# Kernel tuning notes

Hardware: AMD Instinct MI355X
Metric: run time of the kernel (lower is better)

Reference implementation:

```python
import jax, jax.numpy as jnp
import numpy as np

B, C, H, W = 4, 128, 100, 256
M = 2

def setup_inputs() -> dict:
    key = jax.random.key(0)
    ks = jax.random.split(key, 5)
    feat0 = jax.random.normal(ks[0], (B, C, H, W), jnp.float32)
    feat1 = jax.random.normal(ks[1], (B, C, H, W), jnp.float32)
    adapter_weight = jax.random.normal(ks[2], (M, C), jnp.float32)
    # conv: 1x1 Conv2d(M*C -> C); store as [C_out, C_in]
    conv_w = jax.random.normal(ks[3], (C, M * C), jnp.float32) * (1.0 / np.sqrt(M * C))
    conv_b = jnp.zeros((C,), jnp.float32)
    mlp_w = jax.random.normal(ks[4], (C, C), jnp.float32) * (1.0 / np.sqrt(C))
    mlp_b = jnp.zeros((C,), jnp.float32)
    return {"feat0": feat0, "feat1": feat1, "adapter_weight": adapter_weight,
            "conv_w": conv_w, "conv_b": conv_b, "mlp_w": mlp_w, "mlp_b": mlp_b}

def reference(feat0, feat1, adapter_weight, conv_w, conv_b, mlp_w, mlp_b):
    feats = jnp.stack([feat0, feat1], axis=0)              # [M, B, C, H, W]
    b, c, h, w = feat0.shape
    # per-modality scalar-per-channel scale, then concat on channel dim
    scaled = feats * adapter_weight[:, None, :, None, None]
    cat = scaled.transpose(1, 0, 2, 3, 4).reshape(b, -1, h, w)  # [B, M*C, H, W]
    # 1x1 conv == channel matmul
    fused = jnp.einsum('bkhw,ck->bchw', cat, conv_w) + conv_b[None, :, None, None]
    f = fused.transpose(2, 3, 0, 1).reshape(h * w, b, c)   # [(HW), B, C]
    fm = feats.transpose(0, 3, 4, 1, 2).reshape(len(feats), h * w, b, c)  # [M, (HW), B, C]
    # per-location cross-agent attention, summed over modalities
    scores = jnp.einsum('msbc,sdc->msbd', fm, f) / np.sqrt(c).astype(jnp.float32)
    attn = jax.nn.softmax(scores, axis=-1)                 # [M, (HW), B, B]
    retrieved = jnp.einsum('msbd,sdc->sbc', attn, f)       # summed over m
    out = f + jax.nn.relu(retrieved @ mlp_w.T + mlp_b)
    return out.reshape(h, w, b, c).transpose(2, 3, 0, 1)   # [B, C, H, W]
```

## Files before the change

kernel.cpp:

```cpp
#include <hip/hip_runtime.h>

#define HW 25600
#define TS 16
#define NT 1600
#define NB 256

typedef float  f32x4   __attribute__((ext_vector_type(4)));
typedef short  short8  __attribute__((ext_vector_type(8)));
typedef short  short4v __attribute__((ext_vector_type(4)));
typedef unsigned int uint2v __attribute__((ext_vector_type(2)));
typedef unsigned int uint4v __attribute__((ext_vector_type(4)));

__device__ __forceinline__ float bf2f(short h) {
    return __builtin_bit_cast(float, (unsigned)((unsigned short)h) << 16);
}
__device__ __forceinline__ unsigned cvt_pk(float a, float b) {
    unsigned r;
    asm("v_cvt_pk_bf16_f32 %0, %1, %2" : "=v"(r) : "v"(a), "v"(b));
    return r;
}

typedef __attribute__((address_space(3))) const char lds_cchar;
typedef __attribute__((address_space(3))) char lds_char;
typedef __attribute__((address_space(1))) const void g_cvoid;
__device__ __forceinline__ unsigned lds_u32(const void* p) {
    return (unsigned)(uintptr_t)(lds_cchar*)p;
}
__device__ __forceinline__ void dma16(const float* g, unsigned lds_byte) {
    __builtin_amdgcn_global_load_lds(
        (g_cvoid*)g,
        (__attribute__((address_space(3))) void*)(lds_char*)(uintptr_t)lds_byte,
        16, 0, 0);
}

__device__ __forceinline__ short4v tr_read(unsigned a) {
    short4v d;
    asm volatile("ds_read_b64_tr_b16 %0, %1" : "=v"(d) : "v"(a) : "memory");
    return d;
}
__device__ __forceinline__ short4v tr_read128(unsigned a) {
    short4v d;
    asm volatile("ds_read_b64_tr_b16 %0, %1 offset:128" : "=v"(d) : "v"(a) : "memory");
    return d;
}
__device__ __forceinline__ uint4v lds_b128(unsigned a) {
    uint4v d;
    asm volatile("ds_read_b128 %0, %1" : "=v"(d) : "v"(a) : "memory");
    return d;
}
__device__ __forceinline__ void wait_lgkm8() {
    asm volatile("s_waitcnt lgkmcnt(8)" ::: "memory");
    __builtin_amdgcn_sched_barrier(0);
}
__device__ __forceinline__ void wait_lgkm6() {
    asm volatile("s_waitcnt lgkmcnt(6)" ::: "memory");
    __builtin_amdgcn_sched_barrier(0);
}
__device__ __forceinline__ void wait_lgkm4() {
    asm volatile("s_waitcnt lgkmcnt(4)" ::: "memory");
    __builtin_amdgcn_sched_barrier(0);
}
__device__ __forceinline__ void wait_lgkm0() {
    asm volatile("s_waitcnt lgkmcnt(0)" ::: "memory");
    __builtin_amdgcn_sched_barrier(0);
}
__device__ __forceinline__ void wait_vm0() {
    asm volatile("s_waitcnt vmcnt(0)" ::: "memory");
    __builtin_amdgcn_sched_barrier(0);
}
__device__ __forceinline__ void bar_lgkm() {
    asm volatile("s_waitcnt lgkmcnt(0)" ::: "memory");
    __builtin_amdgcn_s_barrier();
    asm volatile("" ::: "memory");
}

struct Clu { short4v lo0, hi0, lo1, hi1, lo2, hi2, lo3, hi3; };
__device__ __forceinline__ void issue_clu(Clu& C, unsigned base, int tstride) {
    C.lo0 = tr_read(base);                C.hi0 = tr_read128(base);
    C.lo1 = tr_read(base + tstride);      C.hi1 = tr_read128(base + tstride);
    C.lo2 = tr_read(base + 2 * tstride);  C.hi2 = tr_read128(base + 2 * tstride);
    C.lo3 = tr_read(base + 3 * tstride);  C.hi3 = tr_read128(base + 3 * tstride);
}
__device__ __forceinline__ short8 mk8(short4v lo, short4v hi) {
    return __builtin_shufflevector(lo, hi, 0, 1, 2, 3, 4, 5, 6, 7);
}

__global__ __launch_bounds__(512, 2) void mmf_kernel(
    const float* __restrict__ feat0, const float* __restrict__ feat1,
    const float* __restrict__ adapter, const float* __restrict__ conv_w,
    const float* __restrict__ conv_b, const float* __restrict__ mlp_w,
    const float* __restrict__ mlp_b, float* __restrict__ out)
{
    __shared__ __align__(128) char smem[133120];
    float* Xf32 = (float*)smem;
    short* Xbf  = (short*)(smem + 65536);
    short* fbf  = (short*)(smem + 98304);
    short* Rbf  = (short*)(smem + 114688);
    float* sc   = (float*)(smem + 131072);

    const int tid = threadIdx.x;
    const int bid = blockIdx.x;
    const int xcd  = bid & 7;
    const int jb   = bid >> 3;
    const int tbeg = 200 * xcd + jb;
    const int tend = 200 * (xcd + 1);
    const int w   = __builtin_amdgcn_readfirstlane(tid >> 6);
    const int l   = tid & 63;
    const int g   = l >> 4;
    const int sl  = l & 15;
    const int c0  = w * 16;

    const unsigned xfbase = lds_u32(Xf32);
    const unsigned xbase  = lds_u32(Xbf);
    const unsigned rbase  = lds_u32(Rbf);

    auto stage_dma = [&](int S) {
        #pragma unroll
        for (int i = 0; i < 8; ++i) {
            int idx = i * 512 + tid;
            int q  = idx & 3;
            int r  = idx >> 2;
            int cc = r & 127;
            int b  = (r >> 7) & 3;
            int m  = r >> 9;
            const float* fp = m ? feat1 : feat0;
            dma16(fp + (size_t)((b * 128 + cc) * HW + S + q * 4),
                  xfbase + (unsigned)((i * 512 + (w << 6)) << 4));
        }
    };

    stage_dma(tbeg * TS);

    short8 afc[8];
    #pragma unroll
    for (int ks = 0; ks < 8; ++ks) {
        const int k0 = ks * 32 + g * 8;
        const float4 w0 = *reinterpret_cast<const float4*>(conv_w + (c0 + sl) * 256 + k0);
        const float4 w1 = *reinterpret_cast<const float4*>(conv_w + (c0 + sl) * 256 + k0 + 4);
        const float4 a0 = *reinterpret_cast<const float4*>(adapter + k0);
        const float4 a1 = *reinterpret_cast<const float4*>(adapter + k0 + 4);
        uint4v au;
        au[0] = cvt_pk(w0.x * a0.x, w0.y * a0.y);
        au[1] = cvt_pk(w0.z * a0.z, w0.w * a0.w);
        au[2] = cvt_pk(w1.x * a1.x, w1.y * a1.y);
        au[3] = cvt_pk(w1.z * a1.z, w1.w * a1.w);
        afc[ks] = __builtin_bit_cast(short8, au);
    }
    short8 afm[4];
    #pragma unroll
    for (int ks = 0; ks < 4; ++ks) {
        const int k0 = ks * 32 + g * 8;
        const float4 w0 = *reinterpret_cast<const float4*>(mlp_w + (c0 + sl) * 128 + k0);
        const float4 w1 = *reinterpret_cast<const float4*>(mlp_w + (c0 + sl) * 128 + k0 + 4);
        uint4v au;
        au[0] = cvt_pk(w0.x, w0.y);
        au[1] = cvt_pk(w0.z, w0.w);
        au[2] = cvt_pk(w1.x, w1.y);
        au[3] = cvt_pk(w1.z, w1.w);
        afm[ks] = __builtin_bit_cast(short8, au);
    }
    float bias[4], mb[4];
    #pragma unroll
    for (int i = 0; i < 4; ++i) {
        bias[i] = conv_b[c0 + g * 4 + i];
        mb[i]   = mlp_b[c0 + g * 4 + i];
    }
    wait_vm0();
    bar_lgkm();

    for (int ti = tbeg; ti < tend; ti += 32) {
        const int S = ti * TS;

        #pragma unroll
        for (int i = 0; i < 8; ++i) {
            int idx = i * 512 + tid;
            const float4 v = *reinterpret_cast<const float4*>(Xf32 + (size_t)idx * 4);
            int q  = idx & 3;
            int r  = idx >> 2;
            int cc = r & 127;
            int b  = (r >> 7) & 3;
            int m  = r >> 9;
            uint2v xv;
            xv[0] = cvt_pk(v.x, v.y);
            xv[1] = cvt_pk(v.z, v.w);
            *reinterpret_cast<uint2v*>(Xbf + b * 4096 + (m * 128 + cc) * 16 + q * 4) = xv;
        }
        bar_lgkm();

        if (ti + 32 < tend) stage_dma((ti + 32) * TS);

        {
            f32x4 acc[4] = {{0,0,0,0},{0,0,0,0},{0,0,0,0},{0,0,0,0}};
            Clu cA, cB;
            issue_clu(cA, xbase + 0 * 1024 + g * 256 + sl * 8, 8192);
            #pragma unroll
            for (int ks = 0; ks < 8; ++ks) {
                Clu& cur = (ks & 1) ? cB : cA;
                Clu& nxt = (ks & 1) ? cA : cB;
                if (ks < 7) {
                    issue_clu(nxt, xbase + (ks + 1) * 1024 + g * 256 + sl * 8, 8192);
                    wait_lgkm8();
                } else {
                    wait_lgkm0();
                }
                acc[0] = __builtin_amdgcn_mfma_f32_16x16x32_bf16(afc[ks], mk8(cur.lo0, cur.hi0), acc[0], 0, 0, 0);
                acc[1] = __builtin_amdgcn_mfma_f32_16x16x32_bf16(afc[ks], mk8(cur.lo1, cur.hi1), acc[1], 0, 0, 0);
                acc[2] = __builtin_amdgcn_mfma_f32_16x16x32_bf16(afc[ks], mk8(cur.lo2, cur.hi2), acc[2], 0, 0, 0);
                acc[3] = __builtin_amdgcn_mfma_f32_16x16x32_bf16(afc[ks], mk8(cur.lo3, cur.hi3), acc[3], 0, 0, 0);
            }
            #pragma unroll
            for (int tt = 0; tt < 4; ++tt) {
                const int col = tt * 16 + sl;
                uint2v fu;
                fu[0] = cvt_pk(acc[tt][0] + bias[0], acc[tt][1] + bias[1]);
                fu[1] = cvt_pk(acc[tt][2] + bias[2], acc[tt][3] + bias[3]);
                *reinterpret_cast<uint2v*>(fbf + col * 128 + (((c0 + g * 4) ^ (sl << 3)) ^ (tt << 5))) = fu;
            }
        }
        bar_lgkm();

        {
            const int sm_m = w >> 2;
            const int sm_b = w & 3;
            const int ad = sl >> 2;
            const int aq = sl & 3;
            const unsigned fbase = lds_u32(fbf);
            const unsigned btile = xbase + sm_b * 8192 + sm_m * 4096 + g * 256 + sl * 8;
            f32x4 accS[4] = {{0,0,0,0},{0,0,0,0},{0,0,0,0},{0,0,0,0}};
            struct SC { short4v blo, bhi; uint4v a0, a1, a2, a3; };
            SC pA, pB;
            auto issue = [&](SC& Sv, int kk) {
                const unsigned bt = btile + (unsigned)(kk * 1024);
                Sv.blo = tr_read(bt); Sv.bhi = tr_read128(bt);
                const int cg = kk * 4 + g;
                Sv.a0 = lds_b128(fbase + (unsigned)((ad * 16 + 0 + aq) * 256 + (((cg ^ (0 + aq)) ^ (ad << 2)) << 4)));
                Sv.a1 = lds_b128(fbase + (unsigned)((ad * 16 + 4 + aq) * 256 + (((cg ^ (4 + aq)) ^ (ad << 2)) << 4)));
                Sv.a2 = lds_b128(fbase + (unsigned)((ad * 16 + 8 + aq) * 256 + (((cg ^ (8 + aq)) ^ (ad << 2)) << 4)));
                Sv.a3 = lds_b128(fbase + (unsigned)((ad * 16 + 12 + aq) * 256 + (((cg ^ (12 + aq)) ^ (ad << 2)) << 4)));
            };
            issue(pA, 0);
            #pragma unroll
            for (int kk = 0; kk < 4; ++kk) {
                SC& cur = (kk & 1) ? pB : pA;
                SC& nxt = (kk & 1) ? pA : pB;
                if (kk < 3) {
                    issue(nxt, kk + 1);
                    wait_lgkm6();
                } else {
                    wait_lgkm0();
                }
                const short8 bf = mk8(cur.blo, cur.bhi);
                accS[0] = __builtin_amdgcn_mfma_f32_16x16x32_bf16(__builtin_bit_cast(short8, cur.a0), bf, accS[0], 0, 0, 0);
                accS[1] = __builtin_amdgcn_mfma_f32_16x16x32_bf16(__builtin_bit_cast(short8, cur.a1), bf, accS[1], 0, 0, 0);
                accS[2] = __builtin_amdgcn_mfma_f32_16x16x32_bf16(__builtin_bit_cast(short8, cur.a2), bf, accS[2], 0, 0, 0);
                accS[3] = __builtin_amdgcn_mfma_f32_16x16x32_bf16(__builtin_bit_cast(short8, cur.a3), bf, accS[3], 0, 0, 0);
            }
            const int cstar = sl >> 2, qstar = sl & 3;
            float x = accS[0][0];
            #pragma unroll
            for (int c = 0; c < 4; ++c)
                #pragma unroll
                for (int q = 0; q < 4; ++q)
                    if (c == cstar && q == qstar) x = accS[c][q];
            x *= 0.088388347648318447f;
            float mx = fmaxf(x, __shfl_xor(x, 16));
            mx = fmaxf(mx, __shfl_xor(mx, 32));
            float e = __expf(x - mx);
            float sm = e + __shfl_xor(e, 16);
            sm += __shfl_xor(sm, 32);
            sc[(sm_m * 16 + sm_b * 4 + g) * 16 + sl] = e / sm;
        }
        bar_lgkm();

        {
            const int b = l >> 4, s = l & 15;
            float aw[4];
            #pragma unroll
            for (int d = 0; d < 4; ++d)
                aw[d] = sc[(b * 4 + d) * 16 + s] + sc[(16 + b * 4 + d) * 16 + s];
            #pragma unroll
            for (int h = 0; h < 2; ++h) {
                const int cb = w * 2 + h;
                float r[8] = {0,0,0,0,0,0,0,0};
                #pragma unroll
                for (int d = 0; d < 4; ++d) {
                    const int colf = d * 16 + s;
                    short8 fv = *reinterpret_cast<const short8*>(
                        fbf + colf * 128 + (((cb ^ s) ^ (d << 2)) << 3));
                    #pragma unroll
                    for (int e = 0; e < 8; ++e) r[e] += aw[d] * bf2f(fv[e]);
                }
                uint4v rv;
                rv[0] = cvt_pk(r[0], r[1]);
                rv[1] = cvt_pk(r[2], r[3]);
                rv[2] = cvt_pk(r[4], r[5]);
                rv[3] = cvt_pk(r[6], r[7]);
                const int v = ((cb ^ s) ^ (b << 2)) & 15;
                *reinterpret_cast<uint4v*>(Rbf + b * 2048 + s * 128 + v * 8) = rv;
            }
        }
        bar_lgkm();

        {
            f32x4 acc[4] = {{0,0,0,0},{0,0,0,0},{0,0,0,0},{0,0,0,0}};
            struct Qu { uint4v q0, q1, q2, q3; };
            Qu qA, qB;
            auto issue_q = [&](Qu& Q, int ks) {
                const unsigned rb = rbase + (unsigned)(sl * 256);
                const int cb = ks * 4 + g;
                Q.q0 = lds_b128(rb + 0 * 4096 + (unsigned)(((cb ^ sl ^ 0) & 15) << 4));
                Q.q1 = lds_b128(rb + 1 * 4096 + (unsigned)(((cb ^ sl ^ 4) & 15) << 4));
                Q.q2 = lds_b128(rb + 2 * 4096 + (unsigned)(((cb ^ sl ^ 8) & 15) << 4));
                Q.q3 = lds_b128(rb + 3 * 4096 + (unsigned)(((cb ^ sl ^ 12) & 15) << 4));
            };
            issue_q(qA, 0);
            #pragma unroll
            for (int ks = 0; ks < 4; ++ks) {
                Qu& cur = (ks & 1) ? qB : qA;
                Qu& nxt = (ks & 1) ? qA : qB;
                if (ks < 3) {
                    issue_q(nxt, ks + 1);
                    wait_lgkm4();
                } else {
                    wait_lgkm0();
                }
                acc[0] = __builtin_amdgcn_mfma_f32_16x16x32_bf16(afm[ks], __builtin_bit_cast(short8, cur.q0), acc[0], 0, 0, 0);
                acc[1] = __builtin_amdgcn_mfma_f32_16x16x32_bf16(afm[ks], __builtin_bit_cast(short8, cur.q1), acc[1], 0, 0, 0);
                acc[2] = __builtin_amdgcn_mfma_f32_16x16x32_bf16(afm[ks], __builtin_bit_cast(short8, cur.q2), acc[2], 0, 0, 0);
                acc[3] = __builtin_amdgcn_mfma_f32_16x16x32_bf16(afm[ks], __builtin_bit_cast(short8, cur.q3), acc[3], 0, 0, 0);
            }
            wait_vm0();
            #pragma unroll
            for (int tt = 0; tt < 4; ++tt) {
                const int col = tt * 16 + sl;
                const short4v res = *reinterpret_cast<const short4v*>(
                    fbf + col * 128 + (((c0 + g * 4) ^ (sl << 3)) ^ (tt << 5)));
                #pragma unroll
                for (int i = 0; i < 4; ++i) {
                    const int c = c0 + g * 4 + i;
                    float v = fmaxf(acc[tt][i] + mb[i], 0.f) + bf2f(res[i]);
                    out[(size_t)(tt * 128 + c) * HW + S + sl] = v;
                }
            }
        }
    }
}

extern "C" void kernel_launch(void* const* d_in, const int* in_sizes, int n_in,
                              void* d_out, int out_size, void* d_ws, size_t ws_size,
                              hipStream_t stream) {
    const float* feat0   = (const float*)d_in[0];
    const float* feat1   = (const float*)d_in[1];
    const float* adapter = (const float*)d_in[2];
    const float* conv_w  = (const float*)d_in[3];
    const float* conv_b  = (const float*)d_in[4];
    const float* mlp_w   = (const float*)d_in[5];
    const float* mlp_b   = (const float*)d_in[6];
    float* out = (float*)d_out;

    dim3 grid(NB);
    dim3 block(512);
    hipLaunchKernelGGL(mmf_kernel, grid, block, 0, stream,
                       feat0, feat1, adapter, conv_w, conv_b, mlp_w, mlp_b, out);
}
```

Measured before the change: 48.71 us.

## Apply MLP to f before attention mixing, dropping retrieved-tensor LDS stage

Uses linearity: instead of computing retrieved = attn·f, writing it to LDS and then multiplying by mlp_w, the kernel multiplies f by mlp_w with MFMA and then mixes the four agent results with the summed attention weights in registers. This removes one LDS write/read pass, one block barrier and the Rbf buffer, which shrinks shared memory. In exchange each thread does 16 extra FMAs per output. Rounding changes slightly because retrieved is no longer rounded to bf16.

```diff
diff --git a/kernel.cpp b/kernel.cpp
--- a/kernel.cpp
+++ b/kernel.cpp
@@ -91,12 +91,11 @@
     const float* __restrict__ conv_b, const float* __restrict__ mlp_w,
     const float* __restrict__ mlp_b, float* __restrict__ out)
 {
-    __shared__ __align__(128) char smem[133120];
+    __shared__ __align__(128) char smem[116736];
     float* Xf32 = (float*)smem;
     short* Xbf  = (short*)(smem + 65536);
     short* fbf  = (short*)(smem + 98304);
-    short* Rbf  = (short*)(smem + 114688);
-    float* sc   = (float*)(smem + 131072);
+    float* sc   = (float*)(smem + 114688);
 
     const int tid = threadIdx.x;
     const int bid = blockIdx.x;
@@ -112,7 +111,7 @@
 
     const unsigned xfbase = lds_u32(Xf32);
     const unsigned xbase  = lds_u32(Xbf);
-    const unsigned rbase  = lds_u32(Rbf);
+    const unsigned fbase  = lds_u32(fbf);
 
     auto stage_dma = [&](int S) {
         #pragma unroll
@@ -224,7 +223,6 @@
             const int sm_b = w & 3;
             const int ad = sl >> 2;
             const int aq = sl & 3;
-            const unsigned fbase = lds_u32(fbf);
             const unsigned btile = xbase + sm_b * 8192 + sm_m * 4096 + g * 256 + sl * 8;
             f32x4 accS[4] = {{0,0,0,0},{0,0,0,0},{0,0,0,0},{0,0,0,0}};
             struct SC { short4v blo, bhi; uint4v a0, a1, a2, a3; };
@@ -273,45 +271,15 @@
         bar_lgkm();
 
         {
-            const int b = l >> 4, s = l & 15;
-            float aw[4];
-            #pragma unroll
-            for (int d = 0; d < 4; ++d)
-                aw[d] = sc[(b * 4 + d) * 16 + s] + sc[(16 + b * 4 + d) * 16 + s];
-            #pragma unroll
-            for (int h = 0; h < 2; ++h) {
-                const int cb = w * 2 + h;
-                float r[8] = {0,0,0,0,0,0,0,0};
-                #pragma unroll
-                for (int d = 0; d < 4; ++d) {
-                    const int colf = d * 16 + s;
-                    short8 fv = *reinterpret_cast<const short8*>(
-                        fbf + colf * 128 + (((cb ^ s) ^ (d << 2)) << 3));
-                    #pragma unroll
-                    for (int e = 0; e < 8; ++e) r[e] += aw[d] * bf2f(fv[e]);
-                }
-                uint4v rv;
-                rv[0] = cvt_pk(r[0], r[1]);
-                rv[1] = cvt_pk(r[2], r[3]);
-                rv[2] = cvt_pk(r[4], r[5]);
-                rv[3] = cvt_pk(r[6], r[7]);
-                const int v = ((cb ^ s) ^ (b << 2)) & 15;
-                *reinterpret_cast<uint4v*>(Rbf + b * 2048 + s * 128 + v * 8) = rv;
-            }
-        }
-        bar_lgkm();
-
-        {
             f32x4 acc[4] = {{0,0,0,0},{0,0,0,0},{0,0,0,0},{0,0,0,0}};
             struct Qu { uint4v q0, q1, q2, q3; };
             Qu qA, qB;
             auto issue_q = [&](Qu& Q, int ks) {
-                const unsigned rb = rbase + (unsigned)(sl * 256);
                 const int cb = ks * 4 + g;
-                Q.q0 = lds_b128(rb + 0 * 4096 + (unsigned)(((cb ^ sl ^ 0) & 15) << 4));
-                Q.q1 = lds_b128(rb + 1 * 4096 + (unsigned)(((cb ^ sl ^ 4) & 15) << 4));
-                Q.q2 = lds_b128(rb + 2 * 4096 + (unsigned)(((cb ^ sl ^ 8) & 15) << 4));
-                Q.q3 = lds_b128(rb + 3 * 4096 + (unsigned)(((cb ^ sl ^ 12) & 15) << 4));
+                Q.q0 = lds_b128(fbase + (unsigned)((0 * 16 + sl) * 256 + (((cb ^ sl) ^ 0)  << 4)));
+                Q.q1 = lds_b128(fbase + (unsigned)((1 * 16 + sl) * 256 + (((cb ^ sl) ^ 4)  << 4)));
+                Q.q2 = lds_b128(fbase + (unsigned)((2 * 16 + sl) * 256 + (((cb ^ sl) ^ 8)  << 4)));
+                Q.q3 = lds_b128(fbase + (unsigned)((3 * 16 + sl) * 256 + (((cb ^ sl) ^ 12) << 4)));
             };
             issue_q(qA, 0);
             #pragma unroll
@@ -329,17 +297,26 @@
                 acc[2] = __builtin_amdgcn_mfma_f32_16x16x32_bf16(afm[ks], __builtin_bit_cast(short8, cur.q2), acc[2], 0, 0, 0);
                 acc[3] = __builtin_amdgcn_mfma_f32_16x16x32_bf16(afm[ks], __builtin_bit_cast(short8, cur.q3), acc[3], 0, 0, 0);
             }
+            float aw_[4][4];
+            #pragma unroll
+            for (int b = 0; b < 4; ++b)
+                #pragma unroll
+                for (int d = 0; d < 4; ++d)
+                    aw_[b][d] = sc[(b * 4 + d) * 16 + sl] + sc[256 + (b * 4 + d) * 16 + sl];
             wait_vm0();
             #pragma unroll
-            for (int tt = 0; tt < 4; ++tt) {
-                const int col = tt * 16 + sl;
+            for (int b = 0; b < 4; ++b) {
+                const int col = b * 16 + sl;
                 const short4v res = *reinterpret_cast<const short4v*>(
-                    fbf + col * 128 + (((c0 + g * 4) ^ (sl << 3)) ^ (tt << 5)));
+                    fbf + col * 128 + (((c0 + g * 4) ^ (sl << 3)) ^ (b << 5)));
                 #pragma unroll
                 for (int i = 0; i < 4; ++i) {
+                    float v = mb[i];
+                    #pragma unroll
+                    for (int d = 0; d < 4; ++d) v += aw_[b][d] * acc[d][i];
                     const int c = c0 + g * 4 + i;
-                    float v = fmaxf(acc[tt][i] + mb[i], 0.f) + bf2f(res[i]);
-                    out[(size_t)(tt * 128 + c) * HW + S + sl] = v;
+                    out[(size_t)(b * 128 + c) * HW + S + sl] =
+                        fmaxf(v, 0.f) + bf2f(res[i]);
                 }
             }
         }
```

Result: faster. 44.73 us (-8.2%).
